# Kernel optimization log

Hardware: AMD Instinct MI355X
Metric: run time of the kernel (lower is better)

Reference implementation:

```python
import jax, jax.numpy as jnp
import numpy as np

N, E, D = 40000, 640000, 128
EPS = 1e-5


def _lin(k, out_d, in_d):
    s = 1.0 / np.sqrt(in_d)
    kw, kb = jax.random.split(k)
    W = jax.random.uniform(kw, (out_d, in_d), minval=-s, maxval=s, dtype=jnp.float32)
    b = jax.random.uniform(kb, (out_d,), minval=-s, maxval=s, dtype=jnp.float32)
    return W, b


def setup_inputs() -> dict:
    key = jax.random.key(0)
    kx, ke, k1, k2, k3, k4 = jax.random.split(key, 6)
    x = jax.random.normal(kx, (N, D), dtype=jnp.float32)
    edge_index = jax.random.randint(ke, (2, E), 0, N, dtype=jnp.int64)
    Wm1, bm1 = _lin(k1, D, D)
    Wm2, bm2 = _lin(k2, D, D)
    Wu1, bu1 = _lin(k3, D, 2 * D)
    Wu2, bu2 = _lin(k4, D, D)
    gamma = jnp.ones((D,), jnp.float32)
    beta = jnp.zeros((D,), jnp.float32)
    return dict(x=x, edge_index=edge_index, Wm1=Wm1, bm1=bm1, Wm2=Wm2, bm2=bm2,
                Wu1=Wu1, bu1=bu1, Wu2=Wu2, bu2=bu2, gamma=gamma, beta=beta)


def reference(x, edge_index, Wm1, bm1, Wm2, bm2, Wu1, bu1, Wu2, bu2, gamma, beta):
    num_nodes = x.shape[0]
    src, dst = edge_index[0], edge_index[1]
    # message MLP on gathered source features: (E, D)
    m = jax.nn.relu(x[src] @ Wm1.T + bm1) @ Wm2.T + bm2
    # scatter-mean via segment_sum + clamped count
    agg = jax.ops.segment_sum(m, dst, num_segments=num_nodes)
    cnt = jax.ops.segment_sum(jnp.ones((dst.shape[0],), m.dtype), dst, num_segments=num_nodes)
    agg = agg / jnp.clip(cnt, 1.0, None)[:, None]
    # update MLP on concat([x, agg]) -> (N, D); dropout is identity in eval
    comb = jnp.concatenate([x, agg], axis=-1)
    u = jax.nn.relu(comb @ Wu1.T + bu1) @ Wu2.T + bu2
    # residual + LayerNorm
    h = u + x
    mu = h.mean(-1, keepdims=True)
    var = ((h - mu) ** 2).mean(-1, keepdims=True)
    return (h - mu) / jnp.sqrt(var + EPS) * gamma + beta
```

## Files before the change

### kernel.cpp

```cpp
#include <hip/hip_runtime.h>

#define N_NODES 40000
#define N_EDGES 640000
#define DIM 128
#define PAD 64
#define NBLK_GEMM 625
#define SCAT_ILP 4
#define SCAT_BLOCKS (N_EDGES / (256 * SCAT_ILP))

typedef __bf16 bf16;
typedef __bf16 v8bf __attribute__((ext_vector_type(8)));
typedef __bf16 v4bf __attribute__((ext_vector_type(4)));
typedef float f32x4 __attribute__((ext_vector_type(4)));

#define MFMA(a, b, c) __builtin_amdgcn_mfma_f32_16x16x32_bf16(a, b, c, 0, 0, 0)

#define OFF_WM1 0
#define OFF_BM1 16384
#define OFF_WM2 16512
#define OFF_BM2 32896
#define OFF_WU1 33024
#define OFF_BU1 65792
#define OFF_WU2 65920
#define OFF_BU2 82304
#define OFF_GAM 82432
#define OFF_BET 82560
#define NPARAM  82688

__device__ __forceinline__ void detect(const void* x, const void* ei,
                                       int* sf, int& f32m, int& i64m) {
    const int tid = threadIdx.x;
    if (tid == 0) { sf[0] = 0; sf[1] = 0; }
    __syncthreads();
    const unsigned short* xh = (const unsigned short*)x;
    const unsigned int* eiw = (const unsigned int*)ei;
    int isf32 = 0; unsigned int orhi = 0;
    #pragma unroll
    for (int j = 0; j < 4; ++j) {
        unsigned short h = xh[2 * (tid + 256 * j)];
        if (((h >> 7) & 0xFF) >= 0xC0) isf32 = 1;
        orhi |= eiw[2 * (tid + 256 * j) + 1];
    }
    if (isf32) atomicOr(&sf[0], 1);
    if (orhi)  atomicOr(&sf[1], 1);
    __syncthreads();
    f32m = sf[0];
    i64m = sf[1] ? 0 : 1;
}

__global__ __launch_bounds__(256) void scatter_kernel(
    const void* __restrict__ x, const void* __restrict__ ei,
    const void* p0, const void* p1, const void* p2, const void* p3,
    const void* p4, const void* p5, const void* p6, const void* p7,
    const void* p8, const void* p9,
    int* __restrict__ cnt, unsigned short* __restrict__ padded,
    bf16* __restrict__ xb, bf16* __restrict__ wp, int* __restrict__ flags)
{
    __shared__ int sf[2];
    int f32m, i64m;
    detect(x, ei, sf, f32m, i64m);
    const int gid = blockIdx.x * 256 + threadIdx.x;
    const int gstride = SCAT_BLOCKS * 256;
    if (gid == 0) { flags[0] = f32m; flags[1] = i64m; }

    int s[SCAT_ILP], d[SCAT_ILP];
    if (i64m) {
        const long long* p = (const long long*)ei;
        #pragma unroll
        for (int j = 0; j < SCAT_ILP; ++j) {
            int e = gid + j * gstride;
            s[j] = (int)p[e]; d[j] = (int)p[N_EDGES + e];
        }
    } else {
        const int* p = (const int*)ei;
        #pragma unroll
        for (int j = 0; j < SCAT_ILP; ++j) {
            int e = gid + j * gstride;
            s[j] = p[e]; d[j] = p[N_EDGES + e];
        }
    }
    int pos[SCAT_ILP];
    #pragma unroll
    for (int j = 0; j < SCAT_ILP; ++j) pos[j] = atomicAdd(&cnt[d[j]], 1);
    #pragma unroll
    for (int j = 0; j < SCAT_ILP; ++j)
        if (pos[j] < PAD) padded[(d[j] << 6) + pos[j]] = (unsigned short)s[j];

    const int NT = N_NODES * DIM;
    if (f32m) {
        const float4* g = (const float4*)x;
        v4bf* o = (v4bf*)xb;
        for (int i = gid; i < NT / 4; i += gstride) {
            float4 v = g[i];
            v4bf t; t[0] = (bf16)v.x; t[1] = (bf16)v.y; t[2] = (bf16)v.z; t[3] = (bf16)v.w;
            o[i] = t;
        }
    } else {
        const uint4* g = (const uint4*)x;
        uint4* o = (uint4*)xb;
        for (int i = gid; i < NT / 8; i += gstride) o[i] = g[i];
    }
    for (int i = gid; i < NPARAM; i += gstride) {
        const void* src; int base;
        if      (i < OFF_BM1) { src = p0; base = OFF_WM1; }
        else if (i < OFF_WM2) { src = p1; base = OFF_BM1; }
        else if (i < OFF_BM2) { src = p2; base = OFF_WM2; }
        else if (i < OFF_WU1) { src = p3; base = OFF_BM2; }
        else if (i < OFF_BU1) { src = p4; base = OFF_WU1; }
        else if (i < OFF_WU2) { src = p5; base = OFF_BU1; }
        else if (i < OFF_BU2) { src = p6; base = OFF_WU2; }
        else if (i < OFF_GAM) { src = p7; base = OFF_BU2; }
        else if (i < OFF_BET) { src = p8; base = OFF_GAM; }
        else                  { src = p9; base = OFF_BET; }
        int j = i - base;
        float v = f32m ? ((const float*)src)[j] : (float)((const bf16*)src)[j];
        wp[i] = (bf16)v;
    }
}

__global__ __launch_bounds__(256) void msg_kernel(const bf16* __restrict__ xb,
                                                  const bf16* __restrict__ wp,
                                                  bf16* __restrict__ y)
{
    __shared__ __align__(16) bf16 sc[4][16 * DIM];
    const int wave = threadIdx.x >> 6, lane = threadIdx.x & 63;
    const int l15 = lane & 15, quad = lane >> 4;
    const int row0 = (blockIdx.x * 4 + wave) * 16;
    bf16* s = sc[wave];
    const size_t ra = (size_t)(row0 + l15) * DIM;

    f32x4 acc[8] = {};
    #pragma unroll
    for (int kt = 0; kt < 4; ++kt) {
        int k0 = kt * 32 + quad * 8;
        v8bf a0 = *(const v8bf*)&xb[ra + k0];
        #pragma unroll
        for (int ct = 0; ct < 8; ++ct) {
            v8bf b = *(const v8bf*)&wp[OFF_WM1 + (size_t)(ct * 16 + l15) * DIM + k0];
            acc[ct] = MFMA(a0, b, acc[ct]);
        }
    }
    #pragma unroll
    for (int ct = 0; ct < 8; ++ct) {
        float bb = (float)wp[OFF_BM1 + ct * 16 + l15];
        int c8w = (ct << 1) | (l15 >> 3);
        #pragma unroll
        for (int r = 0; r < 4; ++r) {
            int row = quad * 4 + r;
            s[row * DIM + (((c8w ^ row) << 3) | (l15 & 7))] =
                (bf16)fmaxf(acc[ct][r] + bb, 0.f);
        }
    }
    f32x4 acc2[8] = {};
    #pragma unroll
    for (int kt = 0; kt < 4; ++kt) {
        int k0 = kt * 32 + quad * 8;
        int c8 = kt * 4 + quad;
        v8bf a0 = *(const v8bf*)&s[l15 * DIM + ((c8 ^ l15) << 3)];
        #pragma unroll
        for (int ct = 0; ct < 8; ++ct) {
            v8bf b = *(const v8bf*)&wp[OFF_WM2 + (size_t)(ct * 16 + l15) * DIM + k0];
            acc2[ct] = MFMA(a0, b, acc2[ct]);
        }
    }
    #pragma unroll
    for (int ct = 0; ct < 8; ++ct) {
        float bb = (float)wp[OFF_BM2 + ct * 16 + l15];
        #pragma unroll
        for (int r = 0; r < 4; ++r) {
            int grow = row0 + quad * 4 + r;
            y[(size_t)grow * DIM + ct * 16 + l15] = (bf16)(acc2[ct][r] + bb);
        }
    }
}

__device__ __forceinline__ void accum8(float* s, uint4 v) {
    v8bf b = __builtin_bit_cast(v8bf, v);
    #pragma unroll
    for (int j = 0; j < 8; ++j) s[j] += (float)b[j];
}

__global__ __launch_bounds__(256) void agg_kernel(const bf16* __restrict__ y,
                                                  const unsigned short* __restrict__ padded,
                                                  const int* __restrict__ cnt,
                                                  bf16* __restrict__ agg) {
    const int node = (blockIdx.x << 2) + (threadIdx.x >> 6);
    const int lane = threadIdx.x & 63;
    const int slot = lane >> 4, c16 = lane & 15;
    const int c = min(cnt[node], PAD);
    const int beg = node << 6;
    const int end = beg + c;
    const uint4* yv = (const uint4*)y;

    float s0[8] = {}, s1[8] = {};
    int e = beg + slot;
    for (; e + 4 < end; e += 8) {
        int i0 = padded[e], i1 = padded[e + 4];
        uint4 v0 = yv[(size_t)i0 * 16 + c16];
        uint4 v1 = yv[(size_t)i1 * 16 + c16];
        accum8(s0, v0);
        accum8(s1, v1);
    }
    if (e < end) accum8(s0, yv[(size_t)padded[e] * 16 + c16]);

    float inv = 1.f / (float)(c > 0 ? c : 1);
    v8bf o;
    #pragma unroll
    for (int j = 0; j < 8; ++j) {
        float v = s0[j] + s1[j];
        v += __shfl_xor(v, 16);
        v += __shfl_xor(v, 32);
        o[j] = (bf16)(v * inv);
    }
    if (slot == 0)
        ((uint4*)agg)[(size_t)node * 16 + c16] = __builtin_bit_cast(uint4, o);
}

__global__ __launch_bounds__(256) void update_kernel(
    const bf16* __restrict__ xb, const bf16* __restrict__ agg,
    const bf16* __restrict__ wp, const int* __restrict__ flags,
    void* __restrict__ out)
{
    __shared__ __align__(16) bf16 sc[4][16 * DIM];
    const int wave = threadIdx.x >> 6, lane = threadIdx.x & 63;
    const int l15 = lane & 15, quad = lane >> 4;
    const int row0 = (blockIdx.x * 4 + wave) * 16;
    bf16* s = sc[wave];
    const size_t ra = (size_t)(row0 + l15) * DIM;
    const int of32 = flags[0];

    f32x4 acc[8] = {};
    #pragma unroll
    for (int kt = 0; kt < 8; ++kt) {
        int k0 = kt * 32 + quad * 8;
        v8bf a0 = (kt < 4) ? *(const v8bf*)&xb[ra + k0]
                           : *(const v8bf*)&agg[ra + (k0 - 128)];
        #pragma unroll
        for (int ct = 0; ct < 8; ++ct) {
            v8bf b = *(const v8bf*)&wp[OFF_WU1 + (size_t)(ct * 16 + l15) * 256 + k0];
            acc[ct] = MFMA(a0, b, acc[ct]);
        }
    }
    #pragma unroll
    for (int ct = 0; ct < 8; ++ct) {
        float bb = (float)wp[OFF_BU1 + ct * 16 + l15];
        int c8w = (ct << 1) | (l15 >> 3);
        #pragma unroll
        for (int r = 0; r < 4; ++r) {
            int row = quad * 4 + r;
            s[row * DIM + (((c8w ^ row) << 3) | (l15 & 7))] =
                (bf16)fmaxf(acc[ct][r] + bb, 0.f);
        }
    }
    f32x4 acc2[8] = {};
    #pragma unroll
    for (int kt = 0; kt < 4; ++kt) {
        int k0 = kt * 32 + quad * 8;
        int c8 = kt * 4 + quad;
        v8bf a0 = *(const v8bf*)&s[l15 * DIM + ((c8 ^ l15) << 3)];
        #pragma unroll
        for (int ct = 0; ct < 8; ++ct) {
            v8bf b = *(const v8bf*)&wp[OFF_WU2 + (size_t)(ct * 16 + l15) * DIM + k0];
            acc2[ct] = MFMA(a0, b, acc2[ct]);
        }
    }

    float bu2c[8], gc[8], bc[8];
    #pragma unroll
    for (int ct = 0; ct < 8; ++ct) {
        int col = ct * 16 + l15;
        bu2c[ct] = (float)wp[OFF_BU2 + col];
        gc[ct]   = (float)wp[OFF_GAM + col];
        bc[ct]   = (float)wp[OFF_BET + col];
    }
    #pragma unroll
    for (int r = 0; r < 4; ++r) {
        int grow = row0 + quad * 4 + r;
        float u[8], s1 = 0.f, s2 = 0.f;
        #pragma unroll
        for (int ct = 0; ct < 8; ++ct) {
            float v = acc2[ct][r] + bu2c[ct]
                    + (float)xb[(size_t)grow * DIM + ct * 16 + l15];
            u[ct] = v; s1 += v; s2 += v * v;
        }
        #pragma unroll
        for (int off = 1; off < 16; off <<= 1) {
            s1 += __shfl_xor(s1, off);
            s2 += __shfl_xor(s2, off);
        }
        float mean = s1 * (1.f / 128.f);
        float var  = s2 * (1.f / 128.f) - mean * mean;
        float rstd = rsqrtf(var + 1e-5f);
        if (of32) {
            #pragma unroll
            for (int ct = 0; ct < 8; ++ct)
                ((float*)out)[(size_t)grow * DIM + ct * 16 + l15] =
                    (u[ct] - mean) * rstd * gc[ct] + bc[ct];
        } else {
            #pragma unroll
            for (int ct = 0; ct < 8; ++ct)
                ((bf16*)out)[(size_t)grow * DIM + ct * 16 + l15] =
                    (bf16)((u[ct] - mean) * rstd * gc[ct] + bc[ct]);
        }
    }
}

extern "C" void kernel_launch(void* const* d_in, const int* in_sizes, int n_in,
                              void* d_out, int out_size, void* d_ws, size_t ws_size,
                              hipStream_t stream) {
    const void* x  = d_in[0];
    const void* ei = d_in[1];

    char* ws = (char*)d_ws;
    size_t off = 0;
    auto alloc = [&](size_t bytes) {
        void* p = ws + off;
        off += (bytes + 255) & ~(size_t)255;
        return p;
    };
    bf16* y   = (bf16*)alloc((size_t)N_NODES * DIM * sizeof(bf16));
    bf16* agg = (bf16*)alloc((size_t)N_NODES * DIM * sizeof(bf16));
    bf16* xb  = (bf16*)alloc((size_t)N_NODES * DIM * sizeof(bf16));
    bf16* wp  = (bf16*)alloc((size_t)NPARAM * sizeof(bf16));
    int*  cnt = (int*)alloc(N_NODES * sizeof(int));
    unsigned short* padded =
        (unsigned short*)alloc((size_t)N_NODES * PAD * sizeof(unsigned short));
    int* flags = (int*)alloc(256);

    hipMemsetAsync(cnt, 0, N_NODES * sizeof(int), stream);

    scatter_kernel<<<SCAT_BLOCKS, 256, 0, stream>>>(
        x, ei, d_in[2], d_in[3], d_in[4], d_in[5], d_in[6], d_in[7],
        d_in[8], d_in[9], d_in[10], d_in[11], cnt, padded, xb, wp, flags);
    msg_kernel<<<NBLK_GEMM, 256, 0, stream>>>(xb, wp, y);
    agg_kernel<<<N_NODES / 4, 256, 0, stream>>>(y, padded, cnt, agg);
    update_kernel<<<NBLK_GEMM, 256, 0, stream>>>(xb, agg, wp, flags, d_out);
}
```

Measured before the change: 227.5 us.

## Fuse neighbor aggregation into update kernel and split edge buckets by class

Removes the separate aggregation kernel and the agg buffer round trip: each update wave now gathers its 16 nodes' neighbor rows into shared memory before the first GEMM. Edge bucketing is split into 8 per-block-class copies (cnt8/pad8) to reduce atomic contention, with edge indices loaded contiguously as int4. Per-class capacity is cut to 32, so the total per node becomes up to 256 slots across classes, and the update kernel pays a prefix walk to locate each edge. The fused gather runs serially over 16 nodes per wave, which lowers parallelism in that phase.

```diff
diff --git a/kernel.cpp b/kernel.cpp
--- a/kernel.cpp
+++ b/kernel.cpp
@@ -3,10 +3,9 @@
 #define N_NODES 40000
 #define N_EDGES 640000
 #define DIM 128
-#define PAD 64
-#define NBLK_GEMM 625
-#define SCAT_ILP 4
-#define SCAT_BLOCKS (N_EDGES / (256 * SCAT_ILP))
+#define PAD 32
+#define NBLK 625
+#define SCAT_BLOCKS 625
 
 typedef __bf16 bf16;
 typedef __bf16 v8bf __attribute__((ext_vector_type(8)));
@@ -53,7 +52,7 @@
     const void* p0, const void* p1, const void* p2, const void* p3,
     const void* p4, const void* p5, const void* p6, const void* p7,
     const void* p8, const void* p9,
-    int* __restrict__ cnt, unsigned short* __restrict__ padded,
+    int* __restrict__ cnt8, unsigned short* __restrict__ pad8,
     bf16* __restrict__ xb, bf16* __restrict__ wp, int* __restrict__ flags)
 {
     __shared__ int sf[2];
@@ -61,30 +60,29 @@
     detect(x, ei, sf, f32m, i64m);
     const int gid = blockIdx.x * 256 + threadIdx.x;
     const int gstride = SCAT_BLOCKS * 256;
+    const int cls = blockIdx.x & 7;
     if (gid == 0) { flags[0] = f32m; flags[1] = i64m; }
 
-    int s[SCAT_ILP], d[SCAT_ILP];
+    int s[4], d[4];
     if (i64m) {
         const long long* p = (const long long*)ei;
-        #pragma unroll
-        for (int j = 0; j < SCAT_ILP; ++j) {
-            int e = gid + j * gstride;
-            s[j] = (int)p[e]; d[j] = (int)p[N_EDGES + e];
-        }
+        int e0 = gid * 4;
+        #pragma unroll
+        for (int j = 0; j < 4; ++j) { s[j] = (int)p[e0 + j]; d[j] = (int)p[N_EDGES + e0 + j]; }
     } else {
-        const int* p = (const int*)ei;
-        #pragma unroll
-        for (int j = 0; j < SCAT_ILP; ++j) {
-            int e = gid + j * gstride;
-            s[j] = p[e]; d[j] = p[N_EDGES + e];
-        }
-    }
-    int pos[SCAT_ILP];
-    #pragma unroll
-    for (int j = 0; j < SCAT_ILP; ++j) pos[j] = atomicAdd(&cnt[d[j]], 1);
-    #pragma unroll
-    for (int j = 0; j < SCAT_ILP; ++j)
-        if (pos[j] < PAD) padded[(d[j] << 6) + pos[j]] = (unsigned short)s[j];
+        const int4* ps = (const int4*)ei;
+        const int4* pd = ps + N_EDGES / 4;
+        int4 sv = ps[gid], dv = pd[gid];
+        s[0] = sv.x; s[1] = sv.y; s[2] = sv.z; s[3] = sv.w;
+        d[0] = dv.x; d[1] = dv.y; d[2] = dv.z; d[3] = dv.w;
+    }
+    int pos[4];
+    #pragma unroll
+    for (int j = 0; j < 4; ++j) pos[j] = atomicAdd(&cnt8[cls * N_NODES + d[j]], 1);
+    #pragma unroll
+    for (int j = 0; j < 4; ++j)
+        if (pos[j] < PAD)
+            pad8[(((size_t)cls * N_NODES + d[j]) << 5) + pos[j]] = (unsigned short)s[j];
 
     const int NT = N_NODES * DIM;
     if (f32m) {
@@ -180,61 +178,79 @@
     for (int j = 0; j < 8; ++j) s[j] += (float)b[j];
 }
 
-__global__ __launch_bounds__(256) void agg_kernel(const bf16* __restrict__ y,
-                                                  const unsigned short* __restrict__ padded,
-                                                  const int* __restrict__ cnt,
-                                                  bf16* __restrict__ agg) {
-    const int node = (blockIdx.x << 2) + (threadIdx.x >> 6);
-    const int lane = threadIdx.x & 63;
-    const int slot = lane >> 4, c16 = lane & 15;
-    const int c = min(cnt[node], PAD);
-    const int beg = node << 6;
-    const int end = beg + c;
-    const uint4* yv = (const uint4*)y;
-
-    float s0[8] = {}, s1[8] = {};
-    int e = beg + slot;
-    for (; e + 4 < end; e += 8) {
-        int i0 = padded[e], i1 = padded[e + 4];
-        uint4 v0 = yv[(size_t)i0 * 16 + c16];
-        uint4 v1 = yv[(size_t)i1 * 16 + c16];
-        accum8(s0, v0);
-        accum8(s1, v1);
-    }
-    if (e < end) accum8(s0, yv[(size_t)padded[e] * 16 + c16]);
-
-    float inv = 1.f / (float)(c > 0 ? c : 1);
-    v8bf o;
-    #pragma unroll
-    for (int j = 0; j < 8; ++j) {
-        float v = s0[j] + s1[j];
-        v += __shfl_xor(v, 16);
-        v += __shfl_xor(v, 32);
-        o[j] = (bf16)(v * inv);
-    }
-    if (slot == 0)
-        ((uint4*)agg)[(size_t)node * 16 + c16] = __builtin_bit_cast(uint4, o);
-}
-
 __global__ __launch_bounds__(256) void update_kernel(
-    const bf16* __restrict__ xb, const bf16* __restrict__ agg,
+    const bf16* __restrict__ xb, const bf16* __restrict__ y,
+    const unsigned short* __restrict__ pad8, const int* __restrict__ cnt8,
     const bf16* __restrict__ wp, const int* __restrict__ flags,
     void* __restrict__ out)
 {
-    __shared__ __align__(16) bf16 sc[4][16 * DIM];
+    __shared__ __align__(16) bf16 sA[4][16 * DIM];
+    __shared__ __align__(16) bf16 sH[4][16 * DIM];
     const int wave = threadIdx.x >> 6, lane = threadIdx.x & 63;
     const int l15 = lane & 15, quad = lane >> 4;
     const int row0 = (blockIdx.x * 4 + wave) * 16;
-    bf16* s = sc[wave];
+    bf16* sa = sA[wave];
+    bf16* s  = sH[wave];
+    const int of32 = flags[0];
+    const uint4* yv = (const uint4*)y;
+
+    for (int idx = 0; idx < 16; ++idx) {
+        const int node = row0 + idx;
+        int pref[9];
+        pref[0] = 0;
+        #pragma unroll
+        for (int xq = 0; xq < 8; ++xq)
+            pref[xq + 1] = pref[xq] + min(cnt8[xq * N_NODES + node], PAD);
+        const int tot = pref[8];
+
+        float s0[8] = {}, s1[8] = {};
+        int j = quad;
+        for (; j + 4 < tot; j += 8) {
+            int j2 = j + 4, x1 = 0, x2 = 0;
+            #pragma unroll
+            for (int xq = 1; xq < 8; ++xq) {
+                if (j  >= pref[xq]) x1 = xq;
+                if (j2 >= pref[xq]) x2 = xq;
+            }
+            int i0 = pad8[(((size_t)x1 * N_NODES + node) << 5) + (j  - pref[x1])];
+            int i1 = pad8[(((size_t)x2 * N_NODES + node) << 5) + (j2 - pref[x2])];
+            uint4 v0 = yv[(size_t)i0 * 16 + l15];
+            uint4 v1 = yv[(size_t)i1 * 16 + l15];
+            accum8(s0, v0);
+            accum8(s1, v1);
+        }
+        if (j < tot) {
+            int x1 = 0;
+            #pragma unroll
+            for (int xq = 1; xq < 8; ++xq) if (j >= pref[xq]) x1 = xq;
+            int i0 = pad8[(((size_t)x1 * N_NODES + node) << 5) + (j - pref[x1])];
+            accum8(s0, yv[(size_t)i0 * 16 + l15]);
+        }
+        float inv = 1.f / (float)(tot > 0 ? tot : 1);
+        v8bf o;
+        #pragma unroll
+        for (int jj = 0; jj < 8; ++jj) {
+            float v = s0[jj] + s1[jj];
+            v += __shfl_xor(v, 16);
+            v += __shfl_xor(v, 32);
+            o[jj] = (bf16)(v * inv);
+        }
+        if (quad == 0)
+            *(v8bf*)&sa[idx * DIM + (((l15 ^ idx) << 3))] = o;
+    }
+
     const size_t ra = (size_t)(row0 + l15) * DIM;
-    const int of32 = flags[0];
-
     f32x4 acc[8] = {};
     #pragma unroll
     for (int kt = 0; kt < 8; ++kt) {
         int k0 = kt * 32 + quad * 8;
-        v8bf a0 = (kt < 4) ? *(const v8bf*)&xb[ra + k0]
-                           : *(const v8bf*)&agg[ra + (k0 - 128)];
+        v8bf a0;
+        if (kt < 4) {
+            a0 = *(const v8bf*)&xb[ra + k0];
+        } else {
+            int c8 = (kt - 4) * 4 + quad;
+            a0 = *(const v8bf*)&sa[l15 * DIM + ((c8 ^ l15) << 3)];
+        }
         #pragma unroll
         for (int ct = 0; ct < 8; ++ct) {
             v8bf b = *(const v8bf*)&wp[OFF_WU1 + (size_t)(ct * 16 + l15) * 256 + k0];
@@ -318,21 +334,19 @@
         off += (bytes + 255) & ~(size_t)255;
         return p;
     };
-    bf16* y   = (bf16*)alloc((size_t)N_NODES * DIM * sizeof(bf16));
-    bf16* agg = (bf16*)alloc((size_t)N_NODES * DIM * sizeof(bf16));
-    bf16* xb  = (bf16*)alloc((size_t)N_NODES * DIM * sizeof(bf16));
-    bf16* wp  = (bf16*)alloc((size_t)NPARAM * sizeof(bf16));
-    int*  cnt = (int*)alloc(N_NODES * sizeof(int));
-    unsigned short* padded =
-        (unsigned short*)alloc((size_t)N_NODES * PAD * sizeof(unsigned short));
+    bf16* y    = (bf16*)alloc((size_t)N_NODES * DIM * sizeof(bf16));
+    bf16* xb   = (bf16*)alloc((size_t)N_NODES * DIM * sizeof(bf16));
+    bf16* wp   = (bf16*)alloc((size_t)NPARAM * sizeof(bf16));
+    int*  cnt8 = (int*)alloc((size_t)8 * N_NODES * sizeof(int));
+    unsigned short* pad8 =
+        (unsigned short*)alloc((size_t)8 * N_NODES * PAD * sizeof(unsigned short));
     int* flags = (int*)alloc(256);
 
-    hipMemsetAsync(cnt, 0, N_NODES * sizeof(int), stream);
+    hipMemsetAsync(cnt8, 0, (size_t)8 * N_NODES * sizeof(int), stream);
 
     scatter_kernel<<<SCAT_BLOCKS, 256, 0, stream>>>(
         x, ei, d_in[2], d_in[3], d_in[4], d_in[5], d_in[6], d_in[7],
-        d_in[8], d_in[9], d_in[10], d_in[11], cnt, padded, xb, wp, flags);
-    msg_kernel<<<NBLK_GEMM, 256, 0, stream>>>(xb, wp, y);
-    agg_kernel<<<N_NODES / 4, 256, 0, stream>>>(y, padded, cnt, agg);
-    update_kernel<<<NBLK_GEMM, 256, 0, stream>>>(xb, agg, wp, flags, d_out);
-}
+        d_in[8], d_in[9], d_in[10], d_in[11], cnt8, pad8, xb, wp, flags);
+    msg_kernel<<<NBLK, 256, 0, stream>>>(xb, wp, y);
+    update_kernel<<<NBLK, 256, 0, stream>>>(xb, y, pad8, cnt8, wp, flags, d_out);
+}
```

New measurement: 232.2 us. +2.0%, slower.
